# Optimization experiments

Measured on AMD Instinct MI355X. Metric: run time of the kernel, lower is better.

## Reference

```python
import jax, jax.numpy as jnp
import numpy as np

B, S, D_MODEL, D_K = 4, 4096, 1024, 64


def setup_inputs() -> dict:
    key = jax.random.key(0)
    ks = jax.random.split(key, 4)
    scale = 1.0 / np.sqrt(D_MODEL)
    x = jax.random.normal(ks[0], (B, S, D_MODEL), dtype=jnp.float32)
    Wq = jax.random.normal(ks[1], (D_MODEL, D_K), dtype=jnp.float32) * scale
    Wk = jax.random.normal(ks[2], (D_MODEL, D_K), dtype=jnp.float32) * scale
    Wv = jax.random.normal(ks[3], (D_MODEL, D_K), dtype=jnp.float32) * scale
    bq = jnp.zeros((D_K,), dtype=jnp.float32)
    bk = jnp.zeros((D_K,), dtype=jnp.float32)
    bv = jnp.zeros((D_K,), dtype=jnp.float32)
    # causal mask: 1 = keep, 0 = masked (matches docstring semantics)
    mask = jnp.broadcast_to(
        jnp.tril(jnp.ones((S, S), dtype=jnp.int32))[None], (B, S, S)
    )
    return {"x": x, "mask": mask, "Wq": Wq, "bq": bq, "Wk": Wk, "bk": bk, "Wv": Wv, "bv": bv}


def reference(x, mask, Wq, bq, Wk, bk, Wv, bv):
    # Q/K/V projections: (B, S, d_model) @ (d_model, d_k) -> (B, S, d_k)
    Q = jnp.einsum("bsd,dk->bsk", x, Wq) + bq
    K = jnp.einsum("bsd,dk->bsk", x, Wk) + bk
    V = jnp.einsum("bsd,dk->bsk", x, Wv) + bv
    # scaled dot-product scores: (B, S, S)
    scores = jnp.einsum("bqk,bsk->bqs", Q, K) / jnp.sqrt(jnp.float32(D_K))
    scores = jnp.where(mask == 0, jnp.float32(-jnp.inf), scores)
    attn = jax.nn.softmax(scores, axis=-1)
    # dropout with p_drop = 0.0 is identity
    out = jnp.einsum("bqs,bsk->bqk", attn, V)  # (B, S, d_k)
    return out
```

## Files before the change

kernel.cpp:

```cpp
#include <hip/hip_runtime.h>
#include <hip/hip_bf16.h>


typedef float  f32x4  __attribute__((ext_vector_type(4)));
typedef float  f32x16 __attribute__((ext_vector_type(16)));
typedef short  s16x8  __attribute__((ext_vector_type(8)));
typedef short  s16x4  __attribute__((ext_vector_type(4)));

#define MFMA16(A, B, C) __builtin_amdgcn_mfma_f32_16x16x32_bf16((A), (B), (C), 0, 0, 0)
#define MFMA32(A, B, C) __builtin_amdgcn_mfma_f32_32x32x16_bf16((A), (B), (C), 0, 0, 0)

#define GLL16(SRC, DST)                                                              \
    __builtin_amdgcn_global_load_lds(                                                \
        (const __attribute__((address_space(1))) unsigned*)(SRC),                    \
        (__attribute__((address_space(3))) unsigned*)(DST), 16, 0, 0)

static __device__ __forceinline__ ushort f2bf(float f) {
    union { float f; unsigned u; } v; v.f = f;
    unsigned u = v.u;
    unsigned r = (u + 0x7FFFu + ((u >> 16) & 1u)) >> 16;
    return (ushort)r;
}

static __device__ __forceinline__ f32x4 fzero() {
    f32x4 v; v[0] = v[1] = v[2] = v[3] = 0.f; return v;
}

__global__ __launch_bounds__(256) void prep_w(const float* __restrict__ Wq,
                                              const float* __restrict__ Wk,
                                              const float* __restrict__ Wv,
                                              short* __restrict__ Wt) {
    const int blk = blockIdx.x;
    const int mat = blk >> 4, kt = blk & 15;
    const float* src = mat == 0 ? Wq : (mat == 1 ? Wk : Wv);
    const float sc = (mat == 0) ? 0.125f : 1.0f;
    __shared__ float wsm[64][68];
    const int t = threadIdx.x;

    const int rb = t >> 4, c4 = (t & 15) * 4;
    #pragma unroll
    for (int i = 0; i < 4; ++i) {
        f32x4 v = *(const f32x4*)&src[(size_t)(kt * 64 + rb + 16 * i) * 64 + c4];
        *(f32x4*)&wsm[rb + 16 * i][c4] = v;
    }
    __syncthreads();

    const int c = t >> 2, ks = (t & 3) * 16;
    s16x8 o0, o1;
    #pragma unroll
    for (int j = 0; j < 8; ++j) o0[j] = (short)f2bf(wsm[ks + j][c] * sc);
    #pragma unroll
    for (int j = 0; j < 8; ++j) o1[j] = (short)f2bf(wsm[ks + 8 + j][c] * sc);
    const size_t ob = (size_t)(mat * 64 + c) * 1024 + kt * 64 + ks;
    *(s16x8*)&Wt[ob]     = o0;
    *(s16x8*)&Wt[ob + 8] = o1;
}

__global__ __launch_bounds__(256, 4) void proj(const float* __restrict__ x,
                                               const short* __restrict__ Wt,
                                               const float* __restrict__ bq,
                                               const float* __restrict__ bk,
                                               const float* __restrict__ bv,
                                               short* __restrict__ Qb,
                                               short* __restrict__ Kb,
                                               short* __restrict__ Vt) {
    const int tid  = threadIdx.x;
    const int lane = tid & 63;
    const int w    = tid >> 6;
    const int m0   = blockIdx.x * 16;
    const int l15  = lane & 15, gr = lane >> 4;

    __shared__ short xs[2][16][136];

    const int srow = tid >> 4;
    const int sc16 = (tid & 15) * 4;
    const float* sbase = x + (size_t)(m0 + srow) * 1024 + sc16;

    f32x4 acc[3];
    #pragma unroll
    for (int m = 0; m < 3; ++m) acc[m] = fzero();

    const short* aptr = Wt + (size_t)(48 * w + l15) * 1024 + 8 * gr;

    f32x4 ld[2];
    ld[0] = *(const f32x4*)(sbase);
    ld[1] = *(const f32x4*)(sbase + 64);
    #pragma unroll
    for (int i = 0; i < 2; ++i) {
        s16x4 o;
        #pragma unroll
        for (int j = 0; j < 4; ++j) o[j] = (short)f2bf(ld[i][j]);
        *(s16x4*)&xs[0][srow][sc16 + 64 * i] = o;
    }

    s16x8 a_cur[3], a_nxt[3];
    #pragma unroll
    for (int m = 0; m < 3; ++m) a_cur[m] = *(const s16x8*)(aptr + (size_t)m * 16 * 1024);
    __syncthreads();

    for (int c = 0; c < 8; ++c) {
        const int buf = c & 1;
        if (c < 7) {
            ld[0] = *(const f32x4*)(sbase + 128 * (c + 1));
            ld[1] = *(const f32x4*)(sbase + 128 * (c + 1) + 64);
        }
        #pragma unroll
        for (int f = 0; f < 4; ++f) {
            const int ko = 128 * c + 32 * f;
            const int kn = (ko + 32) & 1023;
            #pragma unroll
            for (int m = 0; m < 3; ++m) a_nxt[m] = *(const s16x8*)(aptr + (size_t)m * 16 * 1024 + kn);
            s16x8 b = *(const s16x8*)&xs[buf][l15][32 * f + 8 * gr];
            #pragma unroll
            for (int m = 0; m < 3; ++m) acc[m] = MFMA16(a_cur[m], b, acc[m]);
            #pragma unroll
            for (int m = 0; m < 3; ++m) a_cur[m] = a_nxt[m];
        }
        if (c < 7) {
            #pragma unroll
            for (int i = 0; i < 2; ++i) {
                s16x4 o;
                #pragma unroll
                for (int j = 0; j < 4; ++j) o[j] = (short)f2bf(ld[i][j]);
                *(s16x4*)&xs[buf ^ 1][srow][sc16 + 64 * i] = o;
            }
        }
        __syncthreads();
    }

    #pragma unroll
    for (int m = 0; m < 3; ++m) {
        const int c0 = 48 * w + 16 * m + 4 * gr;
        const int row = m0 + l15;
        f32x4 v = acc[m];
        if (c0 < 64) {
            s16x4 o;
            #pragma unroll
            for (int r = 0; r < 4; ++r) o[r] = (short)f2bf(v[r] + 0.125f * bq[c0 + r]);
            *(s16x4*)&Qb[(size_t)row * 64 + c0] = o;
        } else if (c0 < 128) {
            s16x4 o;
            #pragma unroll
            for (int r = 0; r < 4; ++r) o[r] = (short)f2bf(v[r] + bk[c0 - 64 + r]);
            *(s16x4*)&Kb[(size_t)row * 64 + (c0 - 64)] = o;
        } else {
            const int b = row >> 12, s = row & 4095;
            #pragma unroll
            for (int r = 0; r < 4; ++r)
                Vt[((size_t)b * 64 + (c0 - 128 + r)) * 4096 + s] =
                    (short)f2bf(v[r] + bv[c0 - 128 + r]);
        }
    }
}

__global__ __launch_bounds__(256, 3) void attn(const short* __restrict__ Qb,
                                               const short* __restrict__ Kb,
                                               const short* __restrict__ Vt,
                                               float* __restrict__ out) {
    const int bid   = blockIdx.x;
    const int xcd   = bid & 7, bi = bid >> 3;
    const int batch = xcd >> 1;
    const int g     = 127 - 2 * bi - (xcd & 1);
    const int q0    = g * 32;
    const int tid   = threadIdx.x, lane = tid & 63, w = tid >> 6;
    const int l31   = lane & 31, h = lane >> 5, kb = 4 * h;

    __shared__ __align__(16) char smem[32768];
    __shared__ float Mm[4][32], Lm[4][32];

    short* lds_k = (short*)(smem + w * 8192);
    short* lds_v = (short*)(smem + w * 8192 + 4096);
    auto kdst = (__attribute__((address_space(3))) char*)smem + w * 8192;
    auto vdst = kdst + 4096;

    const size_t row0 = (size_t)batch * 4096;
    const short* Kb2 = Kb + row0 * 64;
    const short* Vb2 = Vt + (size_t)batch * 64 * 4096;

    const short* Qp = Qb + (row0 + q0 + l31) * 64 + 8 * h;
    s16x8 qf[4];
    #pragma unroll
    for (int kk = 0; kk < 4; ++kk) qf[kk] = *(const s16x8*)(Qp + 16 * kk);

    f32x16 oT0, oT1;
    #pragma unroll
    for (int r = 0; r < 16; ++r) { oT0[r] = 0.f; oT1[r] = 0.f; }
    float m = -1e30f, l_ = 0.f;

    const int nt = g + 1;
    const int t0 = (nt * w) >> 2, t1 = (nt * (w + 1)) >> 2;

    auto stage = [&](int j0) {
        #pragma unroll
        for (int i = 0; i < 4; ++i) {
            const int s  = 8 * i + (lane >> 3);
            const int cs = ((lane & 7) ^ (s & 7)) * 8;
            GLL16(Kb2 + (size_t)(j0 + s) * 64 + cs, kdst + i * 1024);
        }
        #pragma unroll
        for (int i = 0; i < 4; ++i) {
            const int d  = 16 * i + (lane >> 2);
            const int cs = ((lane & 3) ^ (d & 3)) * 8;
            GLL16(Vb2 + (size_t)d * 4096 + j0 + cs, vdst + i * 1024);
        }
    };

    if (t0 < t1) stage(t0 * 32);

    for (int t = t0; t < t1; ++t) {
        const int j0 = t * 32;

        asm volatile("s_waitcnt vmcnt(0)" ::: "memory");
        __builtin_amdgcn_sched_barrier(0);

        s16x8 kf[4], va[2][2];
        #pragma unroll
        for (int kk = 0; kk < 4; ++kk)
            kf[kk] = *(const s16x8*)(lds_k + l31 * 64 + (((2 * kk + h) ^ (l31 & 7)) * 8));
        #pragma unroll
        for (int dt = 0; dt < 2; ++dt)
            #pragma unroll
            for (int kk = 0; kk < 2; ++kk)
                va[dt][kk] = *(const s16x8*)(lds_v + (32 * dt + l31) * 32 +
                                             (((2 * kk + h) ^ (l31 & 3)) * 8));

        asm volatile("s_waitcnt lgkmcnt(0)" ::: "memory");
        __builtin_amdgcn_sched_barrier(0);
        if (t + 1 < t1) stage(j0 + 32);

        f32x16 sacc;
        #pragma unroll
        for (int r = 0; r < 16; ++r) sacc[r] = 0.f;
        #pragma unroll
        for (int kk = 0; kk < 4; ++kk) sacc = MFMA32(kf[kk], qf[kk], sacc);

        if (j0 == q0) {
            #pragma unroll
            for (int r = 0; r < 16; ++r) {
                const int kvloc = (r & 3) + 8 * (r >> 2) + kb;
                if (kvloc > l31) sacc[r] = -1e30f;
            }
        }

        float tm[8];
        #pragma unroll
        for (int r = 0; r < 8; ++r) tm[r] = fmaxf(sacc[r], sacc[r + 8]);
        #pragma unroll
        for (int r = 0; r < 4; ++r) tm[r] = fmaxf(tm[r], tm[r + 4]);
        tm[0] = fmaxf(fmaxf(tm[0], tm[2]), fmaxf(tm[1], tm[3]));
        float sm = fmaxf(tm[0], __shfl_xor(tm[0], 32));

        if (!__all(sm - m <= 8.f)) {
            const float mn = fmaxf(m, sm);
            const float sc = __expf(m - mn);
            m = mn;
            l_ *= sc;
            #pragma unroll
            for (int r = 0; r < 16; ++r) { oT0[r] *= sc; oT1[r] *= sc; }
        }

        #pragma unroll
        for (int r = 0; r < 16; ++r) sacc[r] = __expf(sacc[r] - m);
        float ts[8];
        #pragma unroll
        for (int r = 0; r < 8; ++r) ts[r] = sacc[r] + sacc[r + 8];
        #pragma unroll
        for (int r = 0; r < 4; ++r) ts[r] = ts[r] + ts[r + 4];
        const float ls = (ts[0] + ts[2]) + (ts[1] + ts[3]);
        l_ += ls + __shfl_xor(ls, 32);

        unsigned pw[8];
        #pragma unroll
        for (int i = 0; i < 8; ++i)
            asm("v_cvt_pk_bf16_f32 %0, %1, %2"
                : "=v"(pw[i]) : "v"(sacc[2 * i]), "v"(sacc[2 * i + 1]));
        asm volatile("v_permlane32_swap_b32 %0, %1" : "+v"(pw[0]), "+v"(pw[2]));
        asm volatile("v_permlane32_swap_b32 %0, %1" : "+v"(pw[1]), "+v"(pw[3]));
        asm volatile("v_permlane32_swap_b32 %0, %1" : "+v"(pw[4]), "+v"(pw[6]));
        asm volatile("v_permlane32_swap_b32 %0, %1" : "+v"(pw[5]), "+v"(pw[7]));
        union { unsigned u[4]; s16x8 v; } f0, f1;
        f0.u[0] = pw[0]; f0.u[1] = pw[1]; f0.u[2] = pw[2]; f0.u[3] = pw[3];
        f1.u[0] = pw[4]; f1.u[1] = pw[5]; f1.u[2] = pw[6]; f1.u[3] = pw[7];

        oT0 = MFMA32(va[0][0], f0.v, oT0);
        oT0 = MFMA32(va[0][1], f1.v, oT0);
        oT1 = MFMA32(va[1][0], f0.v, oT1);
        oT1 = MFMA32(va[1][1], f1.v, oT1);
    }

    asm volatile("s_waitcnt vmcnt(0)" ::: "memory");
    __builtin_amdgcn_sched_barrier(0);

    float* Om_w = (float*)(smem + w * 8192);
    #pragma unroll
    for (int rg = 0; rg < 4; ++rg) {
        f32x4 v0, v1;
        #pragma unroll
        for (int j = 0; j < 4; ++j) { v0[j] = oT0[4 * rg + j]; v1[j] = oT1[4 * rg + j]; }
        const int d0 = rg * 8 + kb;
        *(f32x4*)&Om_w[l31 * 64 + d0]      = v0;
        *(f32x4*)&Om_w[l31 * 64 + 32 + d0] = v1;
    }
    if (lane < 32) { Mm[w][l31] = m; Lm[w][l31] = l_; }
    __syncthreads();

    {
        const int q = tid >> 3, d0 = (tid & 7) * 8;
        const float m0 = Mm[0][q], m1 = Mm[1][q], m2 = Mm[2][q], m3 = Mm[3][q];
        const float mt = fmaxf(fmaxf(m0, m1), fmaxf(m2, m3));
        float sw[4];
        sw[0] = __expf(m0 - mt); sw[1] = __expf(m1 - mt);
        sw[2] = __expf(m2 - mt); sw[3] = __expf(m3 - mt);
        const float lt = sw[0] * Lm[0][q] + sw[1] * Lm[1][q] + sw[2] * Lm[2][q] + sw[3] * Lm[3][q];
        const float inv = 1.f / lt;
        f32x4 a0 = fzero(), a1 = fzero();
        #pragma unroll
        for (int ww = 0; ww < 4; ++ww) {
            const float* Om_r = (const float*)(smem + ww * 8192);
            f32x4 u0 = *(const f32x4*)&Om_r[q * 64 + d0];
            f32x4 u1 = *(const f32x4*)&Om_r[q * 64 + d0 + 4];
            #pragma unroll
            for (int j = 0; j < 4; ++j) { a0[j] += sw[ww] * u0[j]; a1[j] += sw[ww] * u1[j]; }
        }
        const size_t ob = (row0 + q0 + q) * 64 + d0;
        f32x4 r0, r1;
        #pragma unroll
        for (int j = 0; j < 4; ++j) { r0[j] = a0[j] * inv; r1[j] = a1[j] * inv; }
        *(f32x4*)&out[ob]     = r0;
        *(f32x4*)&out[ob + 4] = r1;
    }
}

extern "C" void kernel_launch(void* const* d_in, const int* in_sizes, int n_in,
                              void* d_out, int out_size, void* d_ws, size_t ws_size,
                              hipStream_t stream) {
    const float* x  = (const float*)d_in[0];
    const float* Wq = (const float*)d_in[2];
    const float* bq = (const float*)d_in[3];
    const float* Wk = (const float*)d_in[4];
    const float* bk = (const float*)d_in[5];
    const float* Wv = (const float*)d_in[6];
    const float* bv = (const float*)d_in[7];
    float* out = (float*)d_out;

    char* ws = (char*)d_ws;
    short* Wt = (short*)(ws);
    short* Qb = (short*)(ws + 393216);
    short* Kb = (short*)(ws + 2490368);
    short* Vt = (short*)(ws + 4587520);

    prep_w<<<dim3(48),   dim3(256), 0, stream>>>(Wq, Wk, Wv, Wt);
    proj<<<dim3(1024),   dim3(256), 0, stream>>>(x, Wt, bq, bk, bv, Qb, Kb, Vt);
    attn<<<dim3(512),    dim3(256), 0, stream>>>(Qb, Kb, Vt, out);
}
```

Baseline: 87.50 us.

## Interleave two independent KV streams per wave and deepen projection prefetch

In the attention kernel, each wave splits its KV tile range into two halves and processes them as independent online-softmax streams (A and B) in the same loop iteration, merging them at the end. This doubles the LDS buffers and accumulators and lowers the occupancy target from 3 to 2 blocks per CU, aiming for more instruction-level parallelism between MFMA and exp/reduction work. The projection kernel prefetches x two chunks ahead with a fully unrolled loop to hide global load latency. The cost is more registers and LDS, which reduces occupancy.

```diff
diff --git a/kernel.cpp b/kernel.cpp
--- a/kernel.cpp
+++ b/kernel.cpp
@@ -82,48 +82,54 @@
 
     const short* aptr = Wt + (size_t)(48 * w + l15) * 1024 + 8 * gr;
 
-    f32x4 ld[2];
-    ld[0] = *(const f32x4*)(sbase);
-    ld[1] = *(const f32x4*)(sbase + 64);
-    #pragma unroll
-    for (int i = 0; i < 2; ++i) {
+    f32x4 ldp[2][2];
+    {
+        f32x4 c0a = *(const f32x4*)(sbase);
+        f32x4 c0b = *(const f32x4*)(sbase + 64);
         s16x4 o;
         #pragma unroll
-        for (int j = 0; j < 4; ++j) o[j] = (short)f2bf(ld[i][j]);
-        *(s16x4*)&xs[0][srow][sc16 + 64 * i] = o;
-    }
+        for (int j = 0; j < 4; ++j) o[j] = (short)f2bf(c0a[j]);
+        *(s16x4*)&xs[0][srow][sc16] = o;
+        #pragma unroll
+        for (int j = 0; j < 4; ++j) o[j] = (short)f2bf(c0b[j]);
+        *(s16x4*)&xs[0][srow][sc16 + 64] = o;
+    }
+    ldp[1][0] = *(const f32x4*)(sbase + 128);
+    ldp[1][1] = *(const f32x4*)(sbase + 128 + 64);
+    ldp[0][0] = *(const f32x4*)(sbase + 256);
+    ldp[0][1] = *(const f32x4*)(sbase + 256 + 64);
 
     s16x8 a_cur[3], a_nxt[3];
     #pragma unroll
     for (int m = 0; m < 3; ++m) a_cur[m] = *(const s16x8*)(aptr + (size_t)m * 16 * 1024);
     __syncthreads();
 
+    #pragma unroll
     for (int c = 0; c < 8; ++c) {
-        const int buf = c & 1;
-        if (c < 7) {
-            ld[0] = *(const f32x4*)(sbase + 128 * (c + 1));
-            ld[1] = *(const f32x4*)(sbase + 128 * (c + 1) + 64);
-        }
         #pragma unroll
         for (int f = 0; f < 4; ++f) {
             const int ko = 128 * c + 32 * f;
             const int kn = (ko + 32) & 1023;
             #pragma unroll
             for (int m = 0; m < 3; ++m) a_nxt[m] = *(const s16x8*)(aptr + (size_t)m * 16 * 1024 + kn);
-            s16x8 b = *(const s16x8*)&xs[buf][l15][32 * f + 8 * gr];
+            s16x8 b = *(const s16x8*)&xs[c & 1][l15][32 * f + 8 * gr];
             #pragma unroll
             for (int m = 0; m < 3; ++m) acc[m] = MFMA16(a_cur[m], b, acc[m]);
             #pragma unroll
             for (int m = 0; m < 3; ++m) a_cur[m] = a_nxt[m];
         }
         if (c < 7) {
-            #pragma unroll
-            for (int i = 0; i < 2; ++i) {
-                s16x4 o;
-                #pragma unroll
-                for (int j = 0; j < 4; ++j) o[j] = (short)f2bf(ld[i][j]);
-                *(s16x4*)&xs[buf ^ 1][srow][sc16 + 64 * i] = o;
-            }
+            s16x4 o;
+            #pragma unroll
+            for (int j = 0; j < 4; ++j) o[j] = (short)f2bf(ldp[(c + 1) & 1][0][j]);
+            *(s16x4*)&xs[(c + 1) & 1][srow][sc16] = o;
+            #pragma unroll
+            for (int j = 0; j < 4; ++j) o[j] = (short)f2bf(ldp[(c + 1) & 1][1][j]);
+            *(s16x4*)&xs[(c + 1) & 1][srow][sc16 + 64] = o;
+        }
+        if (c < 5) {
+            ldp[(c + 1) & 1][0] = *(const f32x4*)(sbase + 128 * (c + 3));
+            ldp[(c + 1) & 1][1] = *(const f32x4*)(sbase + 128 * (c + 3) + 64);
         }
         __syncthreads();
     }
@@ -153,7 +159,7 @@
     }
 }
 
-__global__ __launch_bounds__(256, 3) void attn(const short* __restrict__ Qb,
+__global__ __launch_bounds__(256, 2) void attn(const short* __restrict__ Qb,
                                                const short* __restrict__ Kb,
                                                const short* __restrict__ Vt,
                                                float* __restrict__ out) {
@@ -165,13 +171,13 @@
     const int tid   = threadIdx.x, lane = tid & 63, w = tid >> 6;
     const int l31   = lane & 31, h = lane >> 5, kb = 4 * h;
 
-    __shared__ __align__(16) char smem[32768];
+    __shared__ __align__(16) char smem[65536];
     __shared__ float Mm[4][32], Lm[4][32];
 
-    short* lds_k = (short*)(smem + w * 8192);
-    short* lds_v = (short*)(smem + w * 8192 + 4096);
-    auto kdst = (__attribute__((address_space(3))) char*)smem + w * 8192;
-    auto vdst = kdst + 4096;
+    char* baseA = smem + w * 16384;
+    char* baseB = baseA + 8192;
+    short* ldsKA = (short*)baseA;        short* ldsVA = (short*)(baseA + 4096);
+    short* ldsKB = (short*)baseB;        short* ldsVB = (short*)(baseB + 4096);
 
     const size_t row0 = (size_t)batch * 4096;
     const short* Kb2 = Kb + row0 * 64;
@@ -182,15 +188,20 @@
     #pragma unroll
     for (int kk = 0; kk < 4; ++kk) qf[kk] = *(const s16x8*)(Qp + 16 * kk);
 
-    f32x16 oT0, oT1;
-    #pragma unroll
-    for (int r = 0; r < 16; ++r) { oT0[r] = 0.f; oT1[r] = 0.f; }
-    float m = -1e30f, l_ = 0.f;
+    f32x16 oT0A, oT1A, oT0B, oT1B;
+    #pragma unroll
+    for (int r = 0; r < 16; ++r) { oT0A[r] = 0.f; oT1A[r] = 0.f; oT0B[r] = 0.f; oT1B[r] = 0.f; }
+    float mA = -1e30f, lA = 0.f, mB = -1e30f, lB = 0.f;
 
     const int nt = g + 1;
     const int t0 = (nt * w) >> 2, t1 = (nt * (w + 1)) >> 2;
-
-    auto stage = [&](int j0) {
+    const int n  = t1 - t0;
+    const int nA = (n + 1) >> 1, nB = n >> 1;
+    const int tB0 = t0 + nA;
+
+    auto stage = [&](int j0, char* base) {
+        auto kdst = (__attribute__((address_space(3))) char*)base;
+        auto vdst = kdst + 4096;
         #pragma unroll
         for (int i = 0; i < 4; ++i) {
             const int s  = 8 * i + (lane >> 3);
@@ -205,75 +216,191 @@
         }
     };
 
-    if (t0 < t1) stage(t0 * 32);
-
-    for (int t = t0; t < t1; ++t) {
-        const int j0 = t * 32;
+    if (nA > 0) stage(t0 * 32, baseA);
+    if (nB > 0) stage(tB0 * 32, baseB);
+
+    for (int i = 0; i < nB; ++i) {
+        const int jA = (t0 + i) * 32, jB = (tB0 + i) * 32;
 
         asm volatile("s_waitcnt vmcnt(0)" ::: "memory");
         __builtin_amdgcn_sched_barrier(0);
 
-        s16x8 kf[4], va[2][2];
-        #pragma unroll
-        for (int kk = 0; kk < 4; ++kk)
-            kf[kk] = *(const s16x8*)(lds_k + l31 * 64 + (((2 * kk + h) ^ (l31 & 7)) * 8));
+        s16x8 kfA[4], vaA[2][2], kfB[4], vaB[2][2];
+        #pragma unroll
+        for (int kk = 0; kk < 4; ++kk) {
+            const int off = ((2 * kk + h) ^ (l31 & 7)) * 8;
+            kfA[kk] = *(const s16x8*)(ldsKA + l31 * 64 + off);
+            kfB[kk] = *(const s16x8*)(ldsKB + l31 * 64 + off);
+        }
         #pragma unroll
         for (int dt = 0; dt < 2; ++dt)
             #pragma unroll
-            for (int kk = 0; kk < 2; ++kk)
-                va[dt][kk] = *(const s16x8*)(lds_v + (32 * dt + l31) * 32 +
-                                             (((2 * kk + h) ^ (l31 & 3)) * 8));
+            for (int kk = 0; kk < 2; ++kk) {
+                const int off = (32 * dt + l31) * 32 + (((2 * kk + h) ^ (l31 & 3)) * 8);
+                vaA[dt][kk] = *(const s16x8*)(ldsVA + off);
+                vaB[dt][kk] = *(const s16x8*)(ldsVB + off);
+            }
 
         asm volatile("s_waitcnt lgkmcnt(0)" ::: "memory");
         __builtin_amdgcn_sched_barrier(0);
-        if (t + 1 < t1) stage(j0 + 32);
-
-        f32x16 sacc;
-        #pragma unroll
-        for (int r = 0; r < 16; ++r) sacc[r] = 0.f;
-        #pragma unroll
-        for (int kk = 0; kk < 4; ++kk) sacc = MFMA32(kf[kk], qf[kk], sacc);
-
-        if (j0 == q0) {
+        if (i + 1 < nA) stage((t0 + i + 1) * 32, baseA);
+        if (i + 1 < nB) stage((tB0 + i + 1) * 32, baseB);
+
+        f32x16 sA, sB;
+        #pragma unroll
+        for (int r = 0; r < 16; ++r) { sA[r] = 0.f; sB[r] = 0.f; }
+        #pragma unroll
+        for (int kk = 0; kk < 4; ++kk) {
+            sA = MFMA32(kfA[kk], qf[kk], sA);
+            sB = MFMA32(kfB[kk], qf[kk], sB);
+        }
+
+        if (jA == q0) {
             #pragma unroll
             for (int r = 0; r < 16; ++r) {
                 const int kvloc = (r & 3) + 8 * (r >> 2) + kb;
-                if (kvloc > l31) sacc[r] = -1e30f;
+                if (kvloc > l31) sA[r] = -1e30f;
             }
         }
+        if (jB == q0) {
+            #pragma unroll
+            for (int r = 0; r < 16; ++r) {
+                const int kvloc = (r & 3) + 8 * (r >> 2) + kb;
+                if (kvloc > l31) sB[r] = -1e30f;
+            }
+        }
+
+        float tmA[8], tmB[8];
+        #pragma unroll
+        for (int r = 0; r < 8; ++r) { tmA[r] = fmaxf(sA[r], sA[r + 8]); tmB[r] = fmaxf(sB[r], sB[r + 8]); }
+        #pragma unroll
+        for (int r = 0; r < 4; ++r) { tmA[r] = fmaxf(tmA[r], tmA[r + 4]); tmB[r] = fmaxf(tmB[r], tmB[r + 4]); }
+        tmA[0] = fmaxf(fmaxf(tmA[0], tmA[2]), fmaxf(tmA[1], tmA[3]));
+        tmB[0] = fmaxf(fmaxf(tmB[0], tmB[2]), fmaxf(tmB[1], tmB[3]));
+        const float shA = __shfl_xor(tmA[0], 32);
+        const float shB = __shfl_xor(tmB[0], 32);
+        const float smA = fmaxf(tmA[0], shA);
+        const float smB = fmaxf(tmB[0], shB);
+
+        if (!__all(smA - mA <= 8.f)) {
+            const float mn = fmaxf(mA, smA);
+            const float sc = __expf(mA - mn);
+            mA = mn; lA *= sc;
+            #pragma unroll
+            for (int r = 0; r < 16; ++r) { oT0A[r] *= sc; oT1A[r] *= sc; }
+        }
+        if (!__all(smB - mB <= 8.f)) {
+            const float mn = fmaxf(mB, smB);
+            const float sc = __expf(mB - mn);
+            mB = mn; lB *= sc;
+            #pragma unroll
+            for (int r = 0; r < 16; ++r) { oT0B[r] *= sc; oT1B[r] *= sc; }
+        }
+
+        #pragma unroll
+        for (int r = 0; r < 16; ++r) { sA[r] = __expf(sA[r] - mA); sB[r] = __expf(sB[r] - mB); }
+
+        float tsA[8], tsB[8];
+        #pragma unroll
+        for (int r = 0; r < 8; ++r) { tsA[r] = sA[r] + sA[r + 8]; tsB[r] = sB[r] + sB[r + 8]; }
+        #pragma unroll
+        for (int r = 0; r < 4; ++r) { tsA[r] = tsA[r] + tsA[r + 4]; tsB[r] = tsB[r] + tsB[r + 4]; }
+        const float lsA = (tsA[0] + tsA[2]) + (tsA[1] + tsA[3]);
+        const float lsB = (tsB[0] + tsB[2]) + (tsB[1] + tsB[3]);
+        const float lxA = __shfl_xor(lsA, 32);
+        const float lxB = __shfl_xor(lsB, 32);
+        lA += lsA + lxA;
+        lB += lsB + lxB;
+
+        unsigned pwA[8], pwB[8];
+        #pragma unroll
+        for (int i2 = 0; i2 < 8; ++i2) {
+            asm("v_cvt_pk_bf16_f32 %0, %1, %2" : "=v"(pwA[i2]) : "v"(sA[2 * i2]), "v"(sA[2 * i2 + 1]));
+            asm("v_cvt_pk_bf16_f32 %0, %1, %2" : "=v"(pwB[i2]) : "v"(sB[2 * i2]), "v"(sB[2 * i2 + 1]));
+        }
+        asm volatile("v_permlane32_swap_b32 %0, %1" : "+v"(pwA[0]), "+v"(pwA[2]));
+        asm volatile("v_permlane32_swap_b32 %0, %1" : "+v"(pwB[0]), "+v"(pwB[2]));
+        asm volatile("v_permlane32_swap_b32 %0, %1" : "+v"(pwA[1]), "+v"(pwA[3]));
+        asm volatile("v_permlane32_swap_b32 %0, %1" : "+v"(pwB[1]), "+v"(pwB[3]));
+        asm volatile("v_permlane32_swap_b32 %0, %1" : "+v"(pwA[4]), "+v"(pwA[6]));
+        asm volatile("v_permlane32_swap_b32 %0, %1" : "+v"(pwB[4]), "+v"(pwB[6]));
+        asm volatile("v_permlane32_swap_b32 %0, %1" : "+v"(pwA[5]), "+v"(pwA[7]));
+        asm volatile("v_permlane32_swap_b32 %0, %1" : "+v"(pwB[5]), "+v"(pwB[7]));
+        union { unsigned u[4]; s16x8 v; } f0A, f1A, f0B, f1B;
+        f0A.u[0] = pwA[0]; f0A.u[1] = pwA[1]; f0A.u[2] = pwA[2]; f0A.u[3] = pwA[3];
+        f1A.u[0] = pwA[4]; f1A.u[1] = pwA[5]; f1A.u[2] = pwA[6]; f1A.u[3] = pwA[7];
+        f0B.u[0] = pwB[0]; f0B.u[1] = pwB[1]; f0B.u[2] = pwB[2]; f0B.u[3] = pwB[3];
+        f1B.u[0] = pwB[4]; f1B.u[1] = pwB[5]; f1B.u[2] = pwB[6]; f1B.u[3] = pwB[7];
+
+        oT0A = MFMA32(vaA[0][0], f0A.v, oT0A);
+        oT0B = MFMA32(vaB[0][0], f0B.v, oT0B);
+        oT1A = MFMA32(vaA[1][0], f0A.v, oT1A);
+        oT1B = MFMA32(vaB[1][0], f0B.v, oT1B);
+        oT0A = MFMA32(vaA[0][1], f1A.v, oT0A);
+        oT0B = MFMA32(vaB[0][1], f1B.v, oT0B);
+        oT1A = MFMA32(vaA[1][1], f1A.v, oT1A);
+        oT1B = MFMA32(vaB[1][1], f1B.v, oT1B);
+    }
+
+    if (nA > nB) {
+        const int jA = (t0 + nB) * 32;
+        asm volatile("s_waitcnt vmcnt(0)" ::: "memory");
+        __builtin_amdgcn_sched_barrier(0);
+
+        s16x8 kfA[4], vaA[2][2];
+        #pragma unroll
+        for (int kk = 0; kk < 4; ++kk)
+            kfA[kk] = *(const s16x8*)(ldsKA + l31 * 64 + (((2 * kk + h) ^ (l31 & 7)) * 8));
+        #pragma unroll
+        for (int dt = 0; dt < 2; ++dt)
+            #pragma unroll
+            for (int kk = 0; kk < 2; ++kk)
+                vaA[dt][kk] = *(const s16x8*)(ldsVA + (32 * dt + l31) * 32 +
+                                              (((2 * kk + h) ^ (l31 & 3)) * 8));
+
+        f32x16 sA;
+        #pragma unroll
+        for (int r = 0; r < 16; ++r) sA[r] = 0.f;
+        #pragma unroll
+        for (int kk = 0; kk < 4; ++kk) sA = MFMA32(kfA[kk], qf[kk], sA);
+
+        if (jA == q0) {
+            #pragma unroll
+            for (int r = 0; r < 16; ++r) {
+                const int kvloc = (r & 3) + 8 * (r >> 2) + kb;
+                if (kvloc > l31) sA[r] = -1e30f;
+            }
+        }
 
         float tm[8];
         #pragma unroll
-        for (int r = 0; r < 8; ++r) tm[r] = fmaxf(sacc[r], sacc[r + 8]);
+        for (int r = 0; r < 8; ++r) tm[r] = fmaxf(sA[r], sA[r + 8]);
         #pragma unroll
         for (int r = 0; r < 4; ++r) tm[r] = fmaxf(tm[r], tm[r + 4]);
         tm[0] = fmaxf(fmaxf(tm[0], tm[2]), fmaxf(tm[1], tm[3]));
-        float sm = fmaxf(tm[0], __shfl_xor(tm[0], 32));
-
-        if (!__all(sm - m <= 8.f)) {
-            const float mn = fmaxf(m, sm);
-            const float sc = __expf(m - mn);
-            m = mn;
-            l_ *= sc;
-            #pragma unroll
-            for (int r = 0; r < 16; ++r) { oT0[r] *= sc; oT1[r] *= sc; }
-        }
-
-        #pragma unroll
-        for (int r = 0; r < 16; ++r) sacc[r] = __expf(sacc[r] - m);
+        const float sm = fmaxf(tm[0], __shfl_xor(tm[0], 32));
+
+        if (!__all(sm - mA <= 8.f)) {
+            const float mn = fmaxf(mA, sm);
+            const float sc = __expf(mA - mn);
+            mA = mn; lA *= sc;
+            #pragma unroll
+            for (int r = 0; r < 16; ++r) { oT0A[r] *= sc; oT1A[r] *= sc; }
+        }
+        #pragma unroll
+        for (int r = 0; r < 16; ++r) sA[r] = __expf(sA[r] - mA);
         float ts[8];
         #pragma unroll
-        for (int r = 0; r < 8; ++r) ts[r] = sacc[r] + sacc[r + 8];
+        for (int r = 0; r < 8; ++r) ts[r] = sA[r] + sA[r + 8];
         #pragma unroll
         for (int r = 0; r < 4; ++r) ts[r] = ts[r] + ts[r + 4];
         const float ls = (ts[0] + ts[2]) + (ts[1] + ts[3]);
-        l_ += ls + __shfl_xor(ls, 32);
+        lA += ls + __shfl_xor(ls, 32);
 
         unsigned pw[8];
         #pragma unroll
-        for (int i = 0; i < 8; ++i)
-            asm("v_cvt_pk_bf16_f32 %0, %1, %2"
-                : "=v"(pw[i]) : "v"(sacc[2 * i]), "v"(sacc[2 * i + 1]));
+        for (int i2 = 0; i2 < 8; ++i2)
+            asm("v_cvt_pk_bf16_f32 %0, %1, %2" : "=v"(pw[i2]) : "v"(sA[2 * i2]), "v"(sA[2 * i2 + 1]));
         asm volatile("v_permlane32_swap_b32 %0, %1" : "+v"(pw[0]), "+v"(pw[2]));
         asm volatile("v_permlane32_swap_b32 %0, %1" : "+v"(pw[1]), "+v"(pw[3]));
         asm volatile("v_permlane32_swap_b32 %0, %1" : "+v"(pw[4]), "+v"(pw[6]));
@@ -282,26 +409,35 @@
         f0.u[0] = pw[0]; f0.u[1] = pw[1]; f0.u[2] = pw[2]; f0.u[3] = pw[3];
         f1.u[0] = pw[4]; f1.u[1] = pw[5]; f1.u[2] = pw[6]; f1.u[3] = pw[7];
 
-        oT0 = MFMA32(va[0][0], f0.v, oT0);
-        oT0 = MFMA32(va[0][1], f1.v, oT0);
-        oT1 = MFMA32(va[1][0], f0.v, oT1);
-        oT1 = MFMA32(va[1][1], f1.v, oT1);
+        oT0A = MFMA32(vaA[0][0], f0.v, oT0A);
+        oT1A = MFMA32(vaA[1][0], f0.v, oT1A);
+        oT0A = MFMA32(vaA[0][1], f1.v, oT0A);
+        oT1A = MFMA32(vaA[1][1], f1.v, oT1A);
+    }
+
+    const float mT = fmaxf(mA, mB);
+    const float eA = __expf(mA - mT), eB = __expf(mB - mT);
+    const float lT = eA * lA + eB * lB;
+    #pragma unroll
+    for (int r = 0; r < 16; ++r) {
+        oT0A[r] = eA * oT0A[r] + eB * oT0B[r];
+        oT1A[r] = eA * oT1A[r] + eB * oT1B[r];
     }
 
     asm volatile("s_waitcnt vmcnt(0)" ::: "memory");
     __builtin_amdgcn_sched_barrier(0);
 
-    float* Om_w = (float*)(smem + w * 8192);
+    float* Om_w = (float*)(smem + w * 16384);
     #pragma unroll
     for (int rg = 0; rg < 4; ++rg) {
         f32x4 v0, v1;
         #pragma unroll
-        for (int j = 0; j < 4; ++j) { v0[j] = oT0[4 * rg + j]; v1[j] = oT1[4 * rg + j]; }
+        for (int j = 0; j < 4; ++j) { v0[j] = oT0A[4 * rg + j]; v1[j] = oT1A[4 * rg + j]; }
         const int d0 = rg * 8 + kb;
         *(f32x4*)&Om_w[l31 * 64 + d0]      = v0;
         *(f32x4*)&Om_w[l31 * 64 + 32 + d0] = v1;
     }
-    if (lane < 32) { Mm[w][l31] = m; Lm[w][l31] = l_; }
+    if (lane < 32) { Mm[w][l31] = mT; Lm[w][l31] = lT; }
     __syncthreads();
 
     {
@@ -316,7 +452,7 @@
         f32x4 a0 = fzero(), a1 = fzero();
         #pragma unroll
         for (int ww = 0; ww < 4; ++ww) {
-            const float* Om_r = (const float*)(smem + ww * 8192);
+            const float* Om_r = (const float*)(smem + ww * 16384);
             f32x4 u0 = *(const f32x4*)&Om_r[q * 64 + d0];
             f32x4 u1 = *(const f32x4*)&Om_r[q * 64 + d0 + 4];
             #pragma unroll
```

Result: no change. 86.45 us (-1.2%).
